# Optimization experiments

Hardware: AMD Instinct MI355X
Metric: run time of the kernel (lower is better)

The kernel has to match this reference:

```python
import jax, jax.numpy as jnp
import numpy as np

DIM = 1024
HEADS = 8
HEAD_DIM = DIM // HEADS
BASE_DT = 0.1
EPS = 1e-5


def layernorm(t, w, b):
    mu = jnp.mean(t, axis=-1, keepdims=True)
    var = jnp.mean((t - mu) ** 2, axis=-1, keepdims=True)
    return (t - mu) * jax.lax.rsqrt(var + EPS) * w + b


def setup_inputs() -> dict:
    key = jax.random.key(0)
    ks = jax.random.split(key, 9)
    B, L, D = 4, 4096, DIM
    s = 1.0 / np.sqrt(D).astype(np.float32)
    return {
        "x": jax.random.normal(ks[0], (B, L, D), jnp.float32),
        "v": jax.random.normal(ks[1], (B, L, D), jnp.float32),
        "force": jax.random.normal(ks[2], (B, L, D), jnp.float32),
        "norm_x_w": jnp.ones((D,), jnp.float32),
        "norm_x_b": jnp.zeros((D,), jnp.float32),
        "WA": jax.random.uniform(ks[3], (D, D), jnp.float32, -s, s),
        "bA": jax.random.uniform(ks[4], (D,), jnp.float32, -s, s),
        "WB": jax.random.uniform(ks[5], (D, D), jnp.float32, -s, s),
        "bB": jax.random.uniform(ks[6], (D,), jnp.float32, -s, s),
        "Wdt": jax.random.uniform(ks[7], (D, D), jnp.float32, -s, s),
        "bdt": jax.random.uniform(ks[8], (D,), jnp.float32, -s, s),
    }


def _combine(c1, c2):
    # composition of affine maps v -> a*v + b along the sequence
    a1, b1 = c1
    a2, b2 = c2
    return a1 * a2, a2 * b1 + b2


def reference(x, v, force, norm_x_w, norm_x_b, WA, bA, WB, bB, Wdt, bdt):
    # x is normalized but unused downstream (faithful to source); v is unused.
    _ = layernorm(x, norm_x_w, norm_x_b)
    # per-head timescale buffer: 1.5**i repeated head_dim times
    scales = jnp.repeat(1.5 ** jnp.arange(HEADS, dtype=jnp.float32), HEAD_DIM)
    A = jax.nn.sigmoid(force @ WA.T + bA)                      # [B,L,D] decay gates
    dt = jax.nn.softplus(force @ Wdt.T + bdt) * BASE_DT * scales
    B_val = (force @ WB.T + bB) * dt                            # [B,L,D] drive term
    # v_t = A_t * v_{t-1} + B_t via parallel associative scan over seq axis
    _, v_seq = jax.lax.associative_scan(_combine, (A, B_val), axis=1)
    # second scan with A=1 is an exclusive-free prefix sum
    x_seq = jnp.cumsum(v_seq * dt, axis=1)
    return (x_seq, v_seq)
```

## Files before the change

### kernel.cpp

```cpp
#include <hip/hip_runtime.h>
#include <hip/hip_bf16.h>
#include <math.h>


#define BDIM 4
#define LSEQ 4096
#define DDIM 1024
#define MROWS (BDIM*LSEQ)
#define NCH 128
#define CLEN (LSEQ/NCH)
#define N4W (DDIM*DDIM/4)
#define N4F (MROWS*DDIM/4)
#define BK 64

typedef __attribute__((ext_vector_type(8))) unsigned short u16x8;
typedef __attribute__((ext_vector_type(8))) short s16x8;
typedef __attribute__((ext_vector_type(4))) float f32x4;

__device__ inline ushort f2bf(float f) {
    unsigned u = __builtin_bit_cast(unsigned, f);
    unsigned r = (u + 0x7fffu + ((u >> 16) & 1u)) >> 16;
    return (ushort)r;
}
__device__ inline ushort f2h(float f) {
    return __builtin_bit_cast(ushort, (_Float16)f);
}
__device__ inline float h2f(ushort u) {
    return (float)__builtin_bit_cast(_Float16, u);
}

__device__ inline void gld_lds16(const ushort* g, ushort* l) {
    __builtin_amdgcn_global_load_lds(
        (const __attribute__((address_space(1))) void*)g,
        (__attribute__((address_space(3))) void*)l, 16, 0, 0);
}

__global__ void cvt_all(const float* __restrict__ force, const float* __restrict__ wa,
                        const float* __restrict__ wb, const float* __restrict__ wdt,
                        ushort* __restrict__ Fb, ushort* __restrict__ Wcat) {
    int i = blockIdx.x * 256 + threadIdx.x;
    const float* s; ushort* dst; int j;
    if (i < N4F) {
        s = force; dst = Fb; j = i;
    } else {
        int k = i - N4F;
        int w = k >> 18;
        j = k & (N4W - 1);
        s = (w == 0) ? wa : (w == 1) ? wb : wdt;
        dst = Wcat + (size_t)w * DDIM * DDIM;
    }
    float4 v = reinterpret_cast<const float4*>(s)[j];
    ushort4 o;
    o.x = f2bf(v.x); o.y = f2bf(v.y); o.z = f2bf(v.z); o.w = f2bf(v.w);
    reinterpret_cast<ushort4*>(dst)[j] = o;
}

__global__ __launch_bounds__(256) void gemm_fused(
    const ushort* __restrict__ F, const ushort* __restrict__ Wc,
    const float* __restrict__ biasA, const float* __restrict__ biasB,
    const float* __restrict__ biasDt,
    ushort* __restrict__ sA, ushort* __restrict__ sB, ushort* __restrict__ sDt)
{
    __shared__ ushort As[128 * BK];
    __shared__ ushort Bs[128 * BK];
    const int t = threadIdx.x;
    const int bi = blockIdx.x;
    const int bj = blockIdx.y;
    const int lane = t & 63, wid = t >> 6;
    const int wm = wid >> 1, wn = wid & 1;
    const int lr = lane & 15, lg = lane >> 4;
    const int rr = lane >> 3;
    const int cc = lane & 7;

    const size_t aBase = (size_t)bi * 128;
    const size_t bBase = (size_t)bj * 128;

    const ushort* gA[4]; const ushort* gB[4];
    int off[4];
#pragma unroll
    for (int i = 0; i < 4; i++) {
        const int R = i * 32 + wid * 8 + rr;
        const int sw = (cc ^ (R & 7)) * 8;
        gA[i] = F  + (aBase + R) * DDIM + sw;
        gB[i] = Wc + (bBase + R) * DDIM + sw;
        off[i] = (i * 32 + wid * 8) * BK;
    }

    f32x4 acc[4][4] = {};

    for (int k0 = 0; k0 < DDIM; k0 += BK) {
        __syncthreads();
#pragma unroll
        for (int i = 0; i < 4; i++) gld_lds16(gA[i] + k0, &As[off[i]]);
#pragma unroll
        for (int i = 0; i < 4; i++) gld_lds16(gB[i] + k0, &Bs[off[i]]);
        __syncthreads();
#pragma unroll
        for (int kk = 0; kk < 2; kk++) {
            s16x8 af[4], bf[4];
#pragma unroll
            for (int m = 0; m < 4; m++) {
                const int r = wm * 64 + m * 16 + lr;
                const int p = (kk * 4 + lg) ^ (lr & 7);
                af[m] = *reinterpret_cast<const s16x8*>(&As[r * BK + p * 8]);
            }
#pragma unroll
            for (int n = 0; n < 4; n++) {
                const int r = wn * 64 + n * 16 + lr;
                const int p = (kk * 4 + lg) ^ (lr & 7);
                bf[n] = *reinterpret_cast<const s16x8*>(&Bs[r * BK + p * 8]);
            }
#pragma unroll
            for (int m = 0; m < 4; m++)
#pragma unroll
                for (int n = 0; n < 4; n++)
                    acc[m][n] = __builtin_amdgcn_mfma_f32_16x16x32_bf16(af[m], bf[n], acc[m][n], 0, 0, 0);
        }
    }

    const int mat = bj >> 3;
    const int colBase = (bj & 7) * 128 + wn * 64;
    const size_t rowBase = (size_t)bi * 128 + wm * 64;
    const float* bias = (mat == 0) ? biasA : (mat == 1) ? biasB : biasDt;
    ushort* outp = (mat == 0) ? sA : (mat == 1) ? sB : sDt;

#pragma unroll
    for (int n = 0; n < 4; n++) {
        const int d = colBase + n * 16 + lr;
        const float bb = bias[d];
#pragma unroll
        for (int m = 0; m < 4; m++)
#pragma unroll
            for (int r = 0; r < 4; r++) {
                const size_t row = rowBase + m * 16 + lg * 4 + r;
                outp[row * DDIM + d] = f2h(acc[m][n][r] + bb);
            }
    }
}

__device__ inline float sigm(float s) {
    return __builtin_amdgcn_rcpf(1.0f + __expf(-s));
}
__device__ inline float softp(float s) {
    return fmaxf(s, 0.0f) + __logf(1.0f + __expf(-fabsf(s)));
}

__global__ void scan_pass1(const ushort* __restrict__ sA, const ushort* __restrict__ sB,
                           const ushort* __restrict__ sDt, float4* __restrict__ summ)
{
    const int c = blockIdx.x & (NCH - 1);
    const int b = blockIdx.x >> 7;
    const int d4 = threadIdx.x;
    size_t idx4 = ((size_t)b * LSEQ + (size_t)c * CLEN) * (DDIM / 4) + d4;
    const float scl = 0.1f * exp2f(0.58496250072f * (float)(d4 >> 5));
    float a[4] = {1.f,1.f,1.f,1.f}, cc[4] = {}, bv[4] = {}, bx[4] = {};
    for (int i = 0; i < CLEN; i++) {
        ushort4 ua = reinterpret_cast<const ushort4*>(sA)[idx4];
        ushort4 ub = reinterpret_cast<const ushort4*>(sB)[idx4];
        ushort4 ud = reinterpret_cast<const ushort4*>(sDt)[idx4];
        const ushort va[4] = {ua.x, ua.y, ua.z, ua.w};
        const ushort vb[4] = {ub.x, ub.y, ub.z, ub.w};
        const ushort vd[4] = {ud.x, ud.y, ud.z, ud.w};
#pragma unroll
        for (int j = 0; j < 4; j++) {
            const float A  = sigm(h2f(va[j]));
            const float dt = softp(h2f(vd[j])) * scl;
            const float bval = h2f(vb[j]) * dt;
            a[j] *= A;
            cc[j] = fmaf(dt, a[j], cc[j]);
            bv[j] = fmaf(A, bv[j], bval);
            bx[j] = fmaf(dt, bv[j], bx[j]);
        }
        idx4 += DDIM / 4;
    }
    const size_t base = ((size_t)b * NCH + c) * DDIM + (size_t)d4 * 4;
#pragma unroll
    for (int j = 0; j < 4; j++)
        summ[base + j] = make_float4(a[j], cc[j], bv[j], bx[j]);
}

__global__ void scan_pass2(const float4* __restrict__ summ, float2* __restrict__ carry)
{
    const int idx = blockIdx.x * 256 + threadIdx.x;
    const int b = idx >> 10, d = idx & 1023;
    float v = 0.0f, x = 0.0f;
    for (int c = 0; c < NCH; c++) {
        const size_t o = ((size_t)b * NCH + c) * DDIM + d;
        carry[o] = make_float2(v, x);
        float4 s = summ[o];
        x = x + s.y * v + s.w;
        v = s.x * v + s.z;
    }
}

__global__ void scan_pass3(const ushort* __restrict__ sA, const ushort* __restrict__ sB,
                           const ushort* __restrict__ sDt, const float2* __restrict__ carry,
                           float* __restrict__ VS, float* __restrict__ XS)
{
    const int c = blockIdx.x & (NCH - 1);
    const int b = blockIdx.x >> 7;
    const int d4 = threadIdx.x;
    size_t idx4 = ((size_t)b * LSEQ + (size_t)c * CLEN) * (DDIM / 4) + d4;
    const float scl = 0.1f * exp2f(0.58496250072f * (float)(d4 >> 5));
    const size_t cbase = ((size_t)b * NCH + c) * DDIM + (size_t)d4 * 4;
    f32x4 v, x;
#pragma unroll
    for (int j = 0; j < 4; j++) {
        float2 cr = carry[cbase + j];
        v[j] = cr.x; x[j] = cr.y;
    }
    f32x4* VS4 = (f32x4*)VS;
    f32x4* XS4 = (f32x4*)XS;
    for (int i = 0; i < CLEN; i++) {
        ushort4 ua = reinterpret_cast<const ushort4*>(sA)[idx4];
        ushort4 ub = reinterpret_cast<const ushort4*>(sB)[idx4];
        ushort4 ud = reinterpret_cast<const ushort4*>(sDt)[idx4];
        const ushort va[4] = {ua.x, ua.y, ua.z, ua.w};
        const ushort vb[4] = {ub.x, ub.y, ub.z, ub.w};
        const ushort vd[4] = {ud.x, ud.y, ud.z, ud.w};
#pragma unroll
        for (int j = 0; j < 4; j++) {
            const float A  = sigm(h2f(va[j]));
            const float dt = softp(h2f(vd[j])) * scl;
            v[j] = fmaf(A, v[j], h2f(vb[j]) * dt);
            x[j] = fmaf(dt, v[j], x[j]);
        }
        VS4[idx4] = v;
        XS4[idx4] = x;
        idx4 += DDIM / 4;
    }
}

extern "C" void kernel_launch(void* const* d_in, const int* in_sizes, int n_in,
                              void* d_out, int out_size, void* d_ws, size_t ws_size,
                              hipStream_t stream) {
    const float* force = (const float*)d_in[2];
    const float* WA  = (const float*)d_in[5];
    const float* bA  = (const float*)d_in[6];
    const float* WB  = (const float*)d_in[7];
    const float* bB  = (const float*)d_in[8];
    const float* Wdt = (const float*)d_in[9];
    const float* bdt = (const float*)d_in[10];

    float* xseq = (float*)d_out;
    float* vseq = xseq + (size_t)MROWS * DDIM;

    ushort* Fb   = (ushort*)xseq;
    ushort* Wcat = (ushort*)vseq;

    char* ws = (char*)d_ws;
    ushort* sA    = (ushort*) ws;
    ushort* sB    = (ushort*)(ws + ((size_t)32 << 20));
    ushort* sDt   = (ushort*)(ws + ((size_t)64 << 20));
    float4* summ  = (float4*)(ws + ((size_t)96 << 20));
    float2* carry = (float2*)(ws + ((size_t)104 << 20));

    cvt_all<<<(N4F + 3 * N4W) / 256, 256, 0, stream>>>(force, WA, WB, Wdt, Fb, Wcat);

    gemm_fused<<<dim3(128, 24), 256, 0, stream>>>(Fb, Wcat, bA, bB, bdt,
                                                  sA, sB, sDt);

    scan_pass1<<<BDIM * NCH, 256, 0, stream>>>(sA, sB, sDt, summ);
    scan_pass2<<<16, 256, 0, stream>>>(summ, carry);
    scan_pass3<<<BDIM * NCH, 256, 0, stream>>>(sA, sB, sDt, carry, vseq, xseq);
}
```

Baseline: 219.7 us.

## Rewrite GEMM as 256x256-tile, 8-wave, double-buffered pipelined kernel

Replaces the 128x128 single-buffered bf16 MFMA GEMM with a 256x256 output tile per 512-thread block. It uses a 128KB LDS double buffer split into half-tiles and interleaves global->LDS prefetch of the next K slice with MFMA compute using explicit waitcnt, barriers and setprio. It also remaps block IDs with a swizzle for L2 locality. The aim is to hide memory latency and raise arithmetic intensity, at the cost of heavy register and LDS use (one block per CU) and fragile hand-scheduled synchronisation.

```diff
diff --git a/kernel.cpp b/kernel.cpp
--- a/kernel.cpp
+++ b/kernel.cpp
@@ -11,9 +11,7 @@
 #define CLEN (LSEQ/NCH)
 #define N4W (DDIM*DDIM/4)
 #define N4F (MROWS*DDIM/4)
-#define BK 64
-
-typedef __attribute__((ext_vector_type(8))) unsigned short u16x8;
+
 typedef __attribute__((ext_vector_type(8))) short s16x8;
 typedef __attribute__((ext_vector_type(4))) float f32x4;
 
@@ -55,86 +53,147 @@
     reinterpret_cast<ushort4*>(dst)[j] = o;
 }
 
-__global__ __launch_bounds__(256) void gemm_fused(
+
+#define HBASE(HH) ((HH) < 2 ? (HH) * 8192 : 32768 + ((HH) - 2) * 8192)
+
+#define VMW(n) asm volatile("s_waitcnt vmcnt(" #n ")" ::: "memory")
+#define NOVM ((void)0)
+
+#define PHASE(PAR, MG, NG, RDA, DOSTG, HH, TK, VMSTMT)                               \
+  {                                                                                  \
+    if (RDA) {                                                                       \
+      _Pragma("unroll")                                                              \
+      for (int m = 0; m < 4; m++) {                                                  \
+        afr[m][0] = *reinterpret_cast<const s16x8*>(                                 \
+            &S[(PAR) * 16384 + (MG) * 8192 + rdA + m * 1024 + px0]);                 \
+        afr[m][1] = *reinterpret_cast<const s16x8*>(                                 \
+            &S[(PAR) * 16384 + (MG) * 8192 + rdA + m * 1024 + px1]);                 \
+      }                                                                              \
+    }                                                                                \
+    _Pragma("unroll")                                                                \
+    for (int j = 0; j < 2; j++) {                                                    \
+      bfr[j][0] = *reinterpret_cast<const s16x8*>(                                   \
+          &S[32768 + (PAR) * 16384 + (NG) * 8192 + rdB + j * 1024 + px0]);           \
+      bfr[j][1] = *reinterpret_cast<const s16x8*>(                                   \
+          &S[32768 + (PAR) * 16384 + (NG) * 8192 + rdB + j * 1024 + px1]);           \
+    }                                                                                \
+    if (DOSTG) {                                                                     \
+      ushort* d0 = &S[HBASE(HH) + ((TK) & 1) * 16384 + wid * 512];                   \
+      ushort* d1 = &S[HBASE(HH) + ((TK) & 1) * 16384 + 4096 + wid * 512];            \
+      gld_lds16(gsrcs[HH][0] + (TK) * 64, d0);                                       \
+      gld_lds16(gsrcs[HH][1] + (TK) * 64, d1);                                       \
+    }                                                                                \
+    asm volatile("" ::: "memory");                                                   \
+    __builtin_amdgcn_s_barrier();                                                    \
+    asm volatile("s_waitcnt lgkmcnt(0)" ::: "memory");                               \
+    __builtin_amdgcn_sched_barrier(0);                                               \
+    __builtin_amdgcn_s_setprio(1);                                                   \
+    _Pragma("unroll")                                                                \
+    for (int kk = 0; kk < 2; kk++)                                                   \
+      _Pragma("unroll")                                                              \
+      for (int m = 0; m < 4; m++)                                                    \
+        _Pragma("unroll")                                                            \
+        for (int j = 0; j < 2; j++)                                                  \
+          acc[(MG) * 4 + m][(NG) * 2 + j] = __builtin_amdgcn_mfma_f32_16x16x32_bf16( \
+              afr[m][kk], bfr[j][kk], acc[(MG) * 4 + m][(NG) * 2 + j], 0, 0, 0);     \
+    __builtin_amdgcn_s_setprio(0);                                                   \
+    VMSTMT;                                                                          \
+    asm volatile("" ::: "memory");                                                   \
+    __builtin_amdgcn_s_barrier();                                                    \
+    asm volatile("" ::: "memory");                                                   \
+  }
+
+__global__ __launch_bounds__(512) void gemm_fused(
     const ushort* __restrict__ F, const ushort* __restrict__ Wc,
     const float* __restrict__ biasA, const float* __restrict__ biasB,
     const float* __restrict__ biasDt,
     ushort* __restrict__ sA, ushort* __restrict__ sB, ushort* __restrict__ sDt)
 {
-    __shared__ ushort As[128 * BK];
-    __shared__ ushort Bs[128 * BK];
+    __shared__ ushort S[65536];
     const int t = threadIdx.x;
-    const int bi = blockIdx.x;
-    const int bj = blockIdx.y;
+    const int swz = (blockIdx.x & 7) * 96 + (blockIdx.x >> 3);
+    const int bi = swz / 12;
+    const int bj = swz % 12;
     const int lane = t & 63, wid = t >> 6;
-    const int wm = wid >> 1, wn = wid & 1;
+    const int wm = wid >> 2, wn = wid & 3;
     const int lr = lane & 15, lg = lane >> 4;
-    const int rr = lane >> 3;
-    const int cc = lane & 7;
-
-    const size_t aBase = (size_t)bi * 128;
-    const size_t bBase = (size_t)bj * 128;
-
-    const ushort* gA[4]; const ushort* gB[4];
-    int off[4];
-#pragma unroll
-    for (int i = 0; i < 4; i++) {
-        const int R = i * 32 + wid * 8 + rr;
-        const int sw = (cc ^ (R & 7)) * 8;
-        gA[i] = F  + (aBase + R) * DDIM + sw;
-        gB[i] = Wc + (bBase + R) * DDIM + sw;
-        off[i] = (i * 32 + wid * 8) * BK;
-    }
-
-    f32x4 acc[4][4] = {};
-
-    for (int k0 = 0; k0 < DDIM; k0 += BK) {
-        __syncthreads();
-#pragma unroll
-        for (int i = 0; i < 4; i++) gld_lds16(gA[i] + k0, &As[off[i]]);
-#pragma unroll
-        for (int i = 0; i < 4; i++) gld_lds16(gB[i] + k0, &Bs[off[i]]);
-        __syncthreads();
-#pragma unroll
-        for (int kk = 0; kk < 2; kk++) {
-            s16x8 af[4], bf[4];
-#pragma unroll
-            for (int m = 0; m < 4; m++) {
-                const int r = wm * 64 + m * 16 + lr;
-                const int p = (kk * 4 + lg) ^ (lr & 7);
-                af[m] = *reinterpret_cast<const s16x8*>(&As[r * BK + p * 8]);
-            }
-#pragma unroll
-            for (int n = 0; n < 4; n++) {
-                const int r = wn * 64 + n * 16 + lr;
-                const int p = (kk * 4 + lg) ^ (lr & 7);
-                bf[n] = *reinterpret_cast<const s16x8*>(&Bs[r * BK + p * 8]);
-            }
-#pragma unroll
-            for (int m = 0; m < 4; m++)
-#pragma unroll
-                for (int n = 0; n < 4; n++)
-                    acc[m][n] = __builtin_amdgcn_mfma_f32_16x16x32_bf16(af[m], bf[n], acc[m][n], 0, 0, 0);
-        }
-    }
-
-    const int mat = bj >> 3;
-    const int colBase = (bj & 7) * 128 + wn * 64;
-    const size_t rowBase = (size_t)bi * 128 + wm * 64;
+
+    const ushort* gsrcs[4][2];
+#pragma unroll
+    for (int h = 0; h < 2; h++)
+#pragma unroll
+        for (int g = 0; g < 2; g++) {
+            const int R = g * 64 + wid * 8 + (lane >> 3);
+            const int c8 = ((lane & 7) ^ (R & 7)) * 8;
+            gsrcs[h][g]     = F  + ((size_t)(bi * 256 + h * 128 + R)) * DDIM + c8;
+            gsrcs[2 + h][g] = Wc + ((size_t)(bj * 256 + h * 128 + R)) * DDIM + c8;
+        }
+
+    const int rdA = (wm * 64 + lr) * 64;
+    const int rdB = (wn * 32 + lr) * 64;
+    const int px0 = ((0 * 4 + lg) ^ (lr & 7)) * 8;
+    const int px1 = ((1 * 4 + lg) ^ (lr & 7)) * 8;
+
+    f32x4 acc[8][4] = {};
+    s16x8 afr[4][2], bfr[2][2];
+
+    {
+        ushort* d;
+        const int HHo[4] = {0, 2, 3, 1};
+#pragma unroll
+        for (int s_ = 0; s_ < 4; s_++) {
+            const int hh = HHo[s_];
+            const int hb = (hh < 2) ? hh * 8192 : 32768 + (hh - 2) * 8192;
+            d = &S[hb + wid * 512];
+            gld_lds16(gsrcs[hh][0], d);
+            d = &S[hb + 4096 + wid * 512];
+            gld_lds16(gsrcs[hh][1], d);
+        }
+    }
+    VMW(4);
+    asm volatile("" ::: "memory");
+    __builtin_amdgcn_s_barrier();
+    asm volatile("" ::: "memory");
+
+    for (int it = 0; it < 7; ++it) {
+        const int t1 = 2 * it + 1;
+        const int t2 = 2 * it + 2;
+        PHASE(0, 0, 0, 1, 1, 0, t1, VMW(4))
+        PHASE(0, 0, 1, 0, 1, 2, t1, VMW(4))
+        PHASE(0, 1, 0, 1, 1, 3, t1, NOVM)
+        PHASE(0, 1, 1, 0, 1, 1, t1, VMW(4))
+        PHASE(1, 0, 0, 1, 1, 0, t2, VMW(4))
+        PHASE(1, 0, 1, 0, 1, 2, t2, VMW(4))
+        PHASE(1, 1, 0, 1, 1, 3, t2, NOVM)
+        PHASE(1, 1, 1, 0, 1, 1, t2, VMW(4))
+    }
+    PHASE(0, 0, 0, 1, 1, 0, 15, VMW(4))
+    PHASE(0, 0, 1, 0, 1, 2, 15, VMW(4))
+    PHASE(0, 1, 0, 1, 1, 3, 15, NOVM)
+    PHASE(0, 1, 1, 0, 1, 1, 15, VMW(4))
+    PHASE(1, 0, 0, 1, 0, 0, 0,  VMW(2))
+    PHASE(1, 0, 1, 0, 0, 0, 0,  VMW(0))
+    PHASE(1, 1, 0, 1, 0, 0, 0,  NOVM)
+    PHASE(1, 1, 1, 0, 0, 0, 0,  NOVM)
+
+    const int mat = bj >> 2;
     const float* bias = (mat == 0) ? biasA : (mat == 1) ? biasB : biasDt;
     ushort* outp = (mat == 0) ? sA : (mat == 1) ? sB : sDt;
 
 #pragma unroll
-    for (int n = 0; n < 4; n++) {
-        const int d = colBase + n * 16 + lr;
+    for (int ngj = 0; ngj < 4; ngj++) {
+        const int ng = ngj >> 1, j = ngj & 1;
+        const int d = (bj & 3) * 256 + ng * 128 + wn * 32 + j * 16 + lr;
         const float bb = bias[d];
 #pragma unroll
-        for (int m = 0; m < 4; m++)
+        for (int mgm = 0; mgm < 8; mgm++) {
+            const int mg = mgm >> 2, m = mgm & 3;
 #pragma unroll
             for (int r = 0; r < 4; r++) {
-                const size_t row = rowBase + m * 16 + lg * 4 + r;
-                outp[row * DDIM + d] = f2h(acc[m][n][r] + bb);
+                const size_t row = (size_t)bi * 256 + mg * 128 + wm * 64 + m * 16 + lg * 4 + r;
+                outp[row * DDIM + d] = f2h(acc[mgm][ngj][r] + bb);
             }
+        }
     }
 }
 
@@ -257,8 +316,7 @@
 
     cvt_all<<<(N4F + 3 * N4W) / 256, 256, 0, stream>>>(force, WA, WB, Wdt, Fb, Wcat);
 
-    gemm_fused<<<dim3(128, 24), 256, 0, stream>>>(Fb, Wcat, bA, bB, bdt,
-                                                  sA, sB, sDt);
+    gemm_fused<<<768, 512, 0, stream>>>(Fb, Wcat, bA, bB, bdt, sA, sB, sDt);
 
     scan_pass1<<<BDIM * NCH, 256, 0, stream>>>(sA, sB, sDt, summ);
     scan_pass2<<<16, 256, 0, stream>>>(summ, carry);
```

Result: faster. 203.1 us (-7.6%).
